# Optimization experiments

Hardware: AMD Instinct MI355X
Metric: run time of the kernel (lower is better)

## Reference

```python
import jax, jax.numpy as jnp
import numpy as np

N, E, D, H = 50000, 800000, 128, 128


def _uniform_param(key, shape, fan_in):
    bound = 1.0 / np.sqrt(fan_in)
    return jax.random.uniform(key, shape, jnp.float32, -bound, bound)


def setup_inputs() -> dict:
    key = jax.random.key(0)
    ks = jax.random.split(key, 12)
    x = jax.random.normal(ks[0], (N, D), jnp.float32)
    xedge = jax.random.randint(ks[1], (2, E), 0, N, jnp.int64)
    y = jax.random.randint(ks[2], (N,), 0, 2, jnp.int32).astype(bool)
    return {
        "x": x,
        "xedge": xedge,
        "y": y,
        "pretrain": 0,
        # SAGEConv layer 1 (in=D, out=H): lin_l (with bias) applied to mean aggr, lin_r (no bias) to self
        "W1l": _uniform_param(ks[3], (D, H), D),
        "b1l": _uniform_param(ks[4], (H,), D),
        "W1r": _uniform_param(ks[5], (D, H), D),
        # SAGEConv layer 2 (in=H, out=H)
        "W2l": _uniform_param(ks[6], (H, H), H),
        "b2l": _uniform_param(ks[7], (H,), H),
        "W2r": _uniform_param(ks[8], (H, H), H),
        # Decoder weight [H, H]
        "Wdec": _uniform_param(ks[9], (H, H), H),
    }


def sage_conv(h, src, dst, Wl, bl, Wr, num_nodes):
    # gather neighbor features along edges, mean-aggregate by destination
    msgs = h[src]                                            # [E, d]
    agg = jax.ops.segment_sum(msgs, dst, num_segments=num_nodes)
    cnt = jax.ops.segment_sum(jnp.ones((src.shape[0],), h.dtype), dst,
                              num_segments=num_nodes)
    mean = agg / jnp.maximum(cnt, 1.0)[:, None]              # [N, d]
    return mean @ Wl + bl + h @ Wr                           # [N, out]


def reference(x, xedge, y, pretrain, W1l, b1l, W1r, W2l, b2l, W2r, Wdec):
    src, dst = xedge[0], xedge[1]
    n = x.shape[0]
    # Encoder: SAGE = conv1 -> relu -> (dropout: eval identity) -> conv2
    h = jax.nn.relu(sage_conv(x, src, dst, W1l, b1l, W1r, n))
    emb = sage_conv(h, src, dst, W2l, b2l, W2r, n)           # [N, H]
    # Decoder
    dx = emb @ Wdec                                          # [N, H]
    # BCEWithLogits: pos nodes target 1, neg nodes target 0, mean within each group
    ym = y.astype(dx.dtype)                                  # [N]
    n_pos = jnp.sum(ym)
    n_neg = n - n_pos
    hdim = dx.shape[1]
    sp_pos = jax.nn.softplus(-dx)   # bce(logit, 1)
    sp_neg = jax.nn.softplus(dx)    # bce(logit, 0)
    l2 = jnp.sum(sp_pos * ym[:, None]) / (jnp.maximum(n_pos, 1.0) * hdim)
    l1 = jnp.sum(sp_neg * (1.0 - ym)[:, None]) / (jnp.maximum(n_neg, 1.0) * hdim)
    return (l1 + l2, emb)
```

## Files before the change

### kernel.cpp

```cpp
#include <hip/hip_runtime.h>
#include <hip/hip_bf16.h>

#define NDIM 128
#define SCAN_CHUNK 1024

typedef __attribute__((ext_vector_type(8))) short short8;
typedef __attribute__((ext_vector_type(4))) float f32x4;

__device__ __forceinline__ float bf2f(__hip_bfloat16 v) { return __bfloat162float(v); }

__device__ __forceinline__ float ldf(const void* p, long i, int f32) {
    return f32 ? ((const float*)p)[i] : bf2f(((const __hip_bfloat16*)p)[i]);
}
__device__ __forceinline__ void stf(void* p, long i, int f32, float v) {
    if (f32) ((float*)p)[i] = v;
    else     ((__hip_bfloat16*)p)[i] = __float2bfloat16(v);
}
__device__ __forceinline__ short f2bf(float v) {
    __hip_bfloat16 h = __float2bfloat16(v);
    short s;
    __builtin_memcpy(&s, &h, 2);
    return s;
}
__device__ __forceinline__ float bflo(unsigned u) { u <<= 16; float f; __builtin_memcpy(&f, &u, 4); return f; }
__device__ __forceinline__ float bfhi(unsigned u) { u &= 0xffff0000u; float f; __builtin_memcpy(&f, &u, 4); return f; }
__device__ __forceinline__ unsigned packbf(float a, float b) {
    unsigned la = (unsigned short)f2bf(a);
    unsigned hb = (unsigned short)f2bf(b);
    return (hb << 16) | la;
}
__device__ __forceinline__ int aswz(int m, int k) {
    return m * NDIM + ((((k >> 3) ^ (m & 7)) << 3) | (k & 7));
}
__device__ __forceinline__ int wswz(int m, int p) {
    return m * 64 + ((((p >> 2) ^ (m & 7)) << 2) | (p & 3));
}

__global__ void detect_kernel(const int* __restrict__ xedge32,
                              const unsigned int* __restrict__ yw,
                              const unsigned short* __restrict__ xh,
                              int* __restrict__ flags, int* __restrict__ cnt,
                              float* __restrict__ accum, int* __restrict__ npos, int N) {
    const int gid = blockIdx.x * 256 + threadIdx.x;
    for (int i = gid; i < N; i += gridDim.x * 256) cnt[i] = 0;
    if (gid == 0) { accum[0] = 0.f; accum[1] = 0.f; npos[0] = 0; }
    if (blockIdx.x == 0) {
        __shared__ int se, sy, scount;
        const int t = threadIdx.x;
        if (t == 0) { se = 1; sy = 0; scount = 0; }
        __syncthreads();
        for (int i = t; i < 512; i += 256)
            if (xedge32[2 * i + 1] != 0) se = 0;
        for (int i = t; i < 1024; i += 256)
            if (yw[i] > 1u) sy = 1;
        int c = 0;
        for (int i = t; i < 1024; i += 256) {
            int ex = (xh[2 * i] >> 7) & 0xFF;
            if (ex >= 100 && ex <= 150) c++;
        }
        atomicAdd(&scount, c);
        __syncthreads();
        if (t == 0) { flags[0] = se; flags[1] = sy; flags[2] = (scount < 900) ? 1 : 0; }
    }
}


__global__ void prep_kernel(const void* __restrict__ x,
                            const void* __restrict__ W1l, const void* __restrict__ b1l,
                            const void* __restrict__ W1r, const void* __restrict__ W2l,
                            const void* __restrict__ b2l, const void* __restrict__ W2r,
                            const void* __restrict__ Wd, const int* __restrict__ flags,
                            short* __restrict__ T1l, short* __restrict__ T1r,
                            short* __restrict__ T2l, short* __restrict__ T2r,
                            short* __restrict__ Td, float* __restrict__ b1c,
                            float* __restrict__ b2c, unsigned* __restrict__ xb,
                            const int* __restrict__ xedge, int E,
                            int* __restrict__ cnt, int N) {
    const int wf = flags[2];
    const long idx = (long)blockIdx.x * 256 + threadIdx.x;
    if (idx < E) {
        int d = flags[0] ? xedge[2 * (E + idx)] : xedge[E + idx];
        atomicAdd(&cnt[d], 1);
    }
    if (idx < NDIM * NDIM) {
        int k = (int)(idx >> 7), n = (int)(idx & 127);
        int o = n * NDIM + k;
        T1l[o] = f2bf(ldf(W1l, idx, wf));
        T1r[o] = f2bf(ldf(W1r, idx, wf));
        T2l[o] = f2bf(ldf(W2l, idx, wf));
        T2r[o] = f2bf(ldf(W2r, idx, wf));
        Td [o] = f2bf(ldf(Wd , idx, wf));
        if (idx < NDIM) { b1c[idx] = ldf(b1l, idx, wf); b2c[idx] = ldf(b2l, idx, wf); }
    } else {
        long p = idx - NDIM * NDIM;
        long np = (long)N * 64;
        if (p < np) {
            if (wf) {
                float2 v = ((const float2*)x)[p];
                xb[p] = packbf(v.x, v.y);
            } else {
                xb[p] = ((const unsigned*)x)[p];
            }
        }
    }
}


__global__ void scan_partial(const int* __restrict__ cnt, int* __restrict__ bsum, int N) {
    __shared__ int red[256];
    const int t = threadIdx.x;
    const long base = (long)blockIdx.x * SCAN_CHUNK + (long)t * 4;
    int s = 0;
#pragma unroll
    for (int i = 0; i < 4; ++i) { long idx = base + i; if (idx < N) s += cnt[idx]; }
    red[t] = s;
    __syncthreads();
    for (int off = 128; off >= 1; off >>= 1) {
        if (t < off) red[t] += red[t + off];
        __syncthreads();
    }
    if (t == 0) bsum[blockIdx.x] = red[0];
}

__global__ void scan_bsums(const int* __restrict__ bsum, int* __restrict__ boff,
                           int B, int* __restrict__ rowptr, int N) {
    __shared__ int part[1024];
    const int t = threadIdx.x;
    int v = (t < B) ? bsum[t] : 0;
    part[t] = v;
    __syncthreads();
    for (int off = 1; off < 1024; off <<= 1) {
        int u = (t >= off) ? part[t - off] : 0;
        __syncthreads();
        part[t] += u;
        __syncthreads();
    }
    if (t < B) boff[t] = part[t] - v;
    if (t == 1023) rowptr[N] = part[1023];
}

__global__ void scan_scatter(int* __restrict__ cnt, const int* __restrict__ boff,
                             int* __restrict__ rowptr, int N) {
    __shared__ int tsum[256];
    const int t = threadIdx.x;
    const long base = (long)blockIdx.x * SCAN_CHUNK + (long)t * 4;
    int loc[4];
    int s = 0;
#pragma unroll
    for (int i = 0; i < 4; ++i) {
        long idx = base + i;
        int c = (idx < N) ? cnt[idx] : 0;
        loc[i] = s;
        s += c;
    }
    tsum[t] = s;
    __syncthreads();
    for (int off = 1; off < 256; off <<= 1) {
        int u = (t >= off) ? tsum[t - off] : 0;
        __syncthreads();
        tsum[t] += u;
        __syncthreads();
    }
    const int texcl = tsum[t] - s;
    const int b0 = boff[blockIdx.x];
#pragma unroll
    for (int i = 0; i < 4; ++i) {
        long idx = base + i;
        if (idx < N) { rowptr[idx] = b0 + texcl + loc[i]; cnt[idx] = 0; }
    }
}

__global__ void fill_kernel(const int* __restrict__ xedge, int E,
                            const int* __restrict__ flags, const int* __restrict__ rowptr,
                            int* __restrict__ cur, int* __restrict__ col) {
    int e = blockIdx.x * blockDim.x + threadIdx.x;
    if (e >= E) return;
    const int e64 = flags[0];
    int s = e64 ? xedge[2 * e] : xedge[e];
    int d = e64 ? xedge[2 * (E + e)] : xedge[E + e];
    int p = rowptr[d] + atomicAdd(&cur[d], 1);
    col[p] = s;
}


template <bool RELU, int OUTMODE>
__global__ __launch_bounds__(256)
void layer_mfma(const unsigned* __restrict__ Xb, const int* __restrict__ rowptr,
                const int* __restrict__ col, const short* __restrict__ WlT,
                const float* __restrict__ biasc, const short* __restrict__ WrT,
                const short* __restrict__ WdT, const void* __restrict__ yv,
                const int* __restrict__ flags, void* __restrict__ outp,
                float* __restrict__ accum, int* __restrict__ npos, int N) {
    __shared__ short AS[2 * 32 * NDIM];
    __shared__ int ylds[32];
    __shared__ float redm[4][2];
    short* Ms = AS;
    short* Ss = AS + 32 * NDIM;
    unsigned* Msw = (unsigned*)Ms;
    unsigned* Ssw = (unsigned*)Ss;
    const int t = threadIdx.x;
    const int n0 = blockIdx.x * 32;
    const int wf = flags[2];

    if (OUTMODE == 1 && t < 32) {
        const int yb = flags[1];
        int n = n0 + t;
        int yn = -1;
        if (n < N)
            yn = yb ? (int)((const unsigned char*)yv)[n]
                    : (((const int*)yv)[n] != 0 ? 1 : 0);
        ylds[t] = yn;
    }

    {
        const int g = t >> 6, p = t & 63;
        for (int r = g; r < 32; r += 4) {
            int n = n0 + r;
            float m0 = 0.f, m1 = 0.f;
            unsigned su = 0;
            if (n < N) {
                int b = rowptr[n], e = rowptr[n + 1];
                int i = b;
                for (; i + 8 <= e; i += 8) {
                    unsigned u0 = Xb[(long)col[i    ] * 64 + p];
                    unsigned u1 = Xb[(long)col[i + 1] * 64 + p];
                    unsigned u2 = Xb[(long)col[i + 2] * 64 + p];
                    unsigned u3 = Xb[(long)col[i + 3] * 64 + p];
                    unsigned u4 = Xb[(long)col[i + 4] * 64 + p];
                    unsigned u5 = Xb[(long)col[i + 5] * 64 + p];
                    unsigned u6 = Xb[(long)col[i + 6] * 64 + p];
                    unsigned u7 = Xb[(long)col[i + 7] * 64 + p];
                    m0 += ((bflo(u0) + bflo(u1)) + (bflo(u2) + bflo(u3)))
                        + ((bflo(u4) + bflo(u5)) + (bflo(u6) + bflo(u7)));
                    m1 += ((bfhi(u0) + bfhi(u1)) + (bfhi(u2) + bfhi(u3)))
                        + ((bfhi(u4) + bfhi(u5)) + (bfhi(u6) + bfhi(u7)));
                }
                for (; i < e; ++i) {
                    unsigned u = Xb[(long)col[i] * 64 + p];
                    m0 += bflo(u);
                    m1 += bfhi(u);
                }
                float inv = 1.f / fmaxf((float)(e - b), 1.f);
                m0 *= inv; m1 *= inv;
                su = Xb[(long)n * 64 + p];
            }
            int wi = wswz(r, p);
            Msw[wi] = packbf(m0, m1);
            Ssw[wi] = su;
        }
    }
    __syncthreads();
    const int l = t & 63, w = t >> 6;
    const int quad = l >> 4, l15 = l & 15;
    const int wcol = w * 32;
    f32x4 acc[2][2] = {};
    for (int k0 = 0; k0 < NDIM; k0 += 32) {
        const int kc = k0 + quad * 8;
        short8 ams[2], ass[2], bl[2], br[2];
#pragma unroll
        for (int rt = 0; rt < 2; ++rt) {
            int m = rt * 16 + l15;
            ams[rt] = *(const short8*)&Ms[aswz(m, kc)];
            ass[rt] = *(const short8*)&Ss[aswz(m, kc)];
        }
#pragma unroll
        for (int ct = 0; ct < 2; ++ct) {
            int n = wcol + ct * 16 + l15;
            bl[ct] = *(const short8*)&WlT[n * NDIM + kc];
            br[ct] = *(const short8*)&WrT[n * NDIM + kc];
        }
#pragma unroll
        for (int rt = 0; rt < 2; ++rt)
#pragma unroll
            for (int ct = 0; ct < 2; ++ct) {
                acc[rt][ct] = __builtin_amdgcn_mfma_f32_16x16x32_bf16(
                    ams[rt], bl[ct], acc[rt][ct], 0, 0, 0);
                acc[rt][ct] = __builtin_amdgcn_mfma_f32_16x16x32_bf16(
                    ass[rt], br[ct], acc[rt][ct], 0, 0, 0);
            }
    }
    __syncthreads();

    if (OUTMODE == 0) {
#pragma unroll
        for (int ct = 0; ct < 2; ++ct) {
            int cg = wcol + ct * 16 + l15;
            float bv = biasc[cg];
#pragma unroll
            for (int rt = 0; rt < 2; ++rt)
#pragma unroll
                for (int reg = 0; reg < 4; ++reg) {
                    int row = rt * 16 + quad * 4 + reg;
                    float v = acc[rt][ct][reg] + bv;
                    if (RELU) v = fmaxf(v, 0.f);
                    Ms[row * NDIM + cg] = f2bf(v);
                }
        }
        __syncthreads();
        unsigned* ob = (unsigned*)outp;
        for (int idx = t; idx < 2048; idx += 256) {
            int r = idx >> 6;
            if (n0 + r < N) ob[(long)n0 * 64 + idx] = Msw[idx];
        }
    } else {
#pragma unroll
        for (int ct = 0; ct < 2; ++ct) {
            int cg = wcol + ct * 16 + l15;
            float bv = biasc[cg];
#pragma unroll
            for (int rt = 0; rt < 2; ++rt)
#pragma unroll
                for (int reg = 0; reg < 4; ++reg) {
                    int row = rt * 16 + quad * 4 + reg;
                    float v = acc[rt][ct][reg] + bv;
                    Ms[aswz(row, cg)] = f2bf(v);
                    int n = n0 + row;
                    if (n < N) {
                        if (wf) ((float*)outp)[1 + (long)n * NDIM + cg] = v;
                        else ((__hip_bfloat16*)outp)[1 + (long)n * NDIM + cg] =
                                 __float2bfloat16(v);
                    }
                }
        }
        __syncthreads();
        f32x4 acc2[2][2] = {};
        for (int k0 = 0; k0 < NDIM; k0 += 32) {
            const int kc = k0 + quad * 8;
            short8 a[2], b[2];
#pragma unroll
            for (int rt = 0; rt < 2; ++rt)
                a[rt] = *(const short8*)&Ms[aswz(rt * 16 + l15, kc)];
#pragma unroll
            for (int ct = 0; ct < 2; ++ct)
                b[ct] = *(const short8*)&WdT[(wcol + ct * 16 + l15) * NDIM + kc];
#pragma unroll
            for (int rt = 0; rt < 2; ++rt)
#pragma unroll
                for (int ct = 0; ct < 2; ++ct)
                    acc2[rt][ct] = __builtin_amdgcn_mfma_f32_16x16x32_bf16(
                        a[rt], b[ct], acc2[rt][ct], 0, 0, 0);
        }
        float lpos = 0.f, lneg = 0.f;
#pragma unroll
        for (int rt = 0; rt < 2; ++rt)
#pragma unroll
            for (int reg = 0; reg < 4; ++reg) {
                int row = rt * 16 + quad * 4 + reg;
                int yn = ylds[row];
                if (yn >= 0) {
#pragma unroll
                    for (int ct = 0; ct < 2; ++ct) {
                        float z = acc2[rt][ct][reg];
                        float L = log1pf(expf(-fabsf(z)));
                        if (yn) lpos += fmaxf(-z, 0.f) + L;
                        else    lneg += fmaxf(z, 0.f) + L;
                    }
                }
            }
#pragma unroll
        for (int off = 32; off >= 1; off >>= 1) {
            lpos += __shfl_down(lpos, off, 64);
            lneg += __shfl_down(lneg, off, 64);
        }
        if (l == 0) { redm[w][0] = lpos; redm[w][1] = lneg; }
        __syncthreads();
        if (t == 0) {
            atomicAdd(&accum[0], redm[0][0] + redm[1][0] + redm[2][0] + redm[3][0]);
            atomicAdd(&accum[1], redm[0][1] + redm[1][1] + redm[2][1] + redm[3][1]);
            int c = 0;
            for (int i = 0; i < 32; ++i) if (ylds[i] > 0) c++;
            if (c) atomicAdd(npos, c);
        }
    }
}

__global__ void finalize_kernel(const float* __restrict__ accum, const int* __restrict__ npos,
                                const int* __restrict__ flags, void* __restrict__ out, int N) {
    float np_ = (float)(*npos);
    float nn_ = (float)N - np_;
    float l2 = accum[0] / (fmaxf(np_, 1.f) * 128.f);
    float l1 = accum[1] / (fmaxf(nn_, 1.f) * 128.f);
    stf(out, 0, flags[2], l1 + l2);
}


extern "C" void kernel_launch(void* const* d_in, const int* in_sizes, int n_in,
                              void* d_out, int out_size, void* d_ws, size_t ws_size,
                              hipStream_t stream) {
    const void* x    = d_in[0];
    const int* xedge = (const int*)d_in[1];
    const void* y    = d_in[2];
    const void* W1l  = d_in[4];
    const void* b1l  = d_in[5];
    const void* W1r  = d_in[6];
    const void* W2l  = d_in[7];
    const void* b2l  = d_in[8];
    const void* W2r  = d_in[9];
    const void* Wdec = d_in[10];

    const int N = in_sizes[0] / NDIM;
    const int E = in_sizes[1] / 2;

    char* ws = (char*)d_ws;
    size_t off = 0;
    auto alloc = [&](size_t bytes) -> void* {
        void* p = ws + off;
        off = (off + bytes + 255) & ~(size_t)255;
        return p;
    };
    int*   flags  = (int*)alloc(64);
    float* accum  = (float*)alloc(64);
    int*   npos   = (int*)alloc(64);
    int*   bsum   = (int*)alloc(1024 * 4);
    int*   boff   = (int*)alloc(1024 * 4);
    int*   cnt    = (int*)alloc((size_t)N * 4);
    int*   rowptr = (int*)alloc((size_t)(N + 1) * 4);
    int*   col    = (int*)alloc((size_t)E * 4);
    unsigned* xb  = (unsigned*)alloc((size_t)N * 64 * 4);
    unsigned* hbuf = (unsigned*)alloc((size_t)N * 64 * 4);
    short* T1l = (short*)alloc(NDIM * NDIM * 2);
    short* T1r = (short*)alloc(NDIM * NDIM * 2);
    short* T2l = (short*)alloc(NDIM * NDIM * 2);
    short* T2r = (short*)alloc(NDIM * NDIM * 2);
    short* Td  = (short*)alloc(NDIM * NDIM * 2);
    float* b1c = (float*)alloc(NDIM * 4);
    float* b2c = (float*)alloc(NDIM * 4);

    const int zb = (N + 255) / 256;
    detect_kernel<<<zb, 256, 0, stream>>>(xedge, (const unsigned int*)y,
                                          (const unsigned short*)x, flags, cnt,
                                          accum, npos, N);
    const long prep_items = (long)NDIM * NDIM + (long)N * 64;
    prep_kernel<<<(int)((prep_items + 255) / 256), 256, 0, stream>>>(
        x, W1l, b1l, W1r, W2l, b2l, W2r, Wdec, flags,
        T1l, T1r, T2l, T2r, Td, b1c, b2c, xb, xedge, E, cnt, N);

    const int sb = (N + SCAN_CHUNK - 1) / SCAN_CHUNK;
    scan_partial<<<sb, 256, 0, stream>>>(cnt, bsum, N);
    scan_bsums<<<1, 1024, 0, stream>>>(bsum, boff, sb, rowptr, N);
    scan_scatter<<<sb, 256, 0, stream>>>(cnt, boff, rowptr, N);

    const int eb = (E + 255) / 256;
    fill_kernel<<<eb, 256, 0, stream>>>(xedge, E, flags, rowptr, cnt, col);

    const int nb32 = (N + 31) / 32;
    layer_mfma<true, 0><<<nb32, 256, 0, stream>>>(
        xb, rowptr, col, T1l, b1c, T1r, nullptr, nullptr, flags,
        hbuf, nullptr, nullptr, N);
    layer_mfma<false, 1><<<nb32, 256, 0, stream>>>(
        hbuf, rowptr, col, T2l, b2c, T2r, Td, y, flags,
        d_out, accum, npos, N);
    finalize_kernel<<<1, 1, 0, stream>>>(accum, npos, flags, d_out, N);
}
```

Before: 369.2 us.

## Batch neighbor gathers with wave-wide column prefetch and skip bf16 input copy

Each wave now loads up to 32 neighbor column indices in one vector load and broadcasts them with readlane, issuing 32 independent feature gathers per row (clamped duplicates for short rows) before reducing under a degree mask. The next row's rowptr and column indices are prefetched while the current row is being summed. When inputs are already bf16, the prep copy of x is skipped and the layer reads the raw input directly. The aim is more memory-level parallelism and less index-load latency in the aggregation, at the cost of higher register use and redundant loads for low-degree nodes.

After: 329.4 us. -10.8%, faster.

```diff
diff --git a/kernel.cpp b/kernel.cpp
--- a/kernel.cpp
+++ b/kernel.cpp
@@ -2,6 +2,7 @@
 #include <hip/hip_bf16.h>
 
 #define NDIM 128
+#define MROWS 32
 #define SCAN_CHUNK 1024
 
 typedef __attribute__((ext_vector_type(8))) short short8;
@@ -91,16 +92,12 @@
         T2r[o] = f2bf(ldf(W2r, idx, wf));
         Td [o] = f2bf(ldf(Wd , idx, wf));
         if (idx < NDIM) { b1c[idx] = ldf(b1l, idx, wf); b2c[idx] = ldf(b2l, idx, wf); }
-    } else {
+    } else if (wf) {
         long p = idx - NDIM * NDIM;
         long np = (long)N * 64;
         if (p < np) {
-            if (wf) {
-                float2 v = ((const float2*)x)[p];
-                xb[p] = packbf(v.x, v.y);
-            } else {
-                xb[p] = ((const unsigned*)x)[p];
-            }
+            float2 v = ((const float2*)x)[p];
+            xb[p] = packbf(v.x, v.y);
         }
     }
 }
@@ -185,24 +182,26 @@
 
 template <bool RELU, int OUTMODE>
 __global__ __launch_bounds__(256)
-void layer_mfma(const unsigned* __restrict__ Xb, const int* __restrict__ rowptr,
+void layer_mfma(const unsigned* __restrict__ Xb, const unsigned* __restrict__ Xraw,
+                const int* __restrict__ rowptr,
                 const int* __restrict__ col, const short* __restrict__ WlT,
                 const float* __restrict__ biasc, const short* __restrict__ WrT,
                 const short* __restrict__ WdT, const void* __restrict__ yv,
                 const int* __restrict__ flags, void* __restrict__ outp,
                 float* __restrict__ accum, int* __restrict__ npos, int N) {
-    __shared__ short AS[2 * 32 * NDIM];
-    __shared__ int ylds[32];
+    __shared__ short AS[2 * MROWS * NDIM];
+    __shared__ int ylds[MROWS];
     __shared__ float redm[4][2];
     short* Ms = AS;
-    short* Ss = AS + 32 * NDIM;
+    short* Ss = AS + MROWS * NDIM;
     unsigned* Msw = (unsigned*)Ms;
     unsigned* Ssw = (unsigned*)Ss;
     const int t = threadIdx.x;
-    const int n0 = blockIdx.x * 32;
+    const int n0 = blockIdx.x * MROWS;
     const int wf = flags[2];
-
-    if (OUTMODE == 1 && t < 32) {
+    const unsigned* __restrict__ X = wf ? Xb : Xraw;
+
+    if (OUTMODE == 1 && t < MROWS) {
         const int yb = flags[1];
         int n = n0 + t;
         int yn = -1;
@@ -213,40 +212,77 @@
     }
 
     {
-        const int g = t >> 6, p = t & 63;
-        for (int r = g; r < 32; r += 4) {
+        const int p = t & 63;
+        const int lj = t & 31;
+        const int g = __builtin_amdgcn_readfirstlane(t >> 6);
+        int r = g;
+        int b = 0, e = 0;
+        {
             int n = n0 + r;
+            if (n < N) {
+                b = __builtin_amdgcn_readfirstlane(rowptr[n]);
+                e = __builtin_amdgcn_readfirstlane(rowptr[n + 1]);
+            }
+        }
+        unsigned colv = 0;
+        if (e > b) {
+            int cl = b + lj;
+            if (cl >= e) cl = e - 1;
+            colv = (unsigned)col[cl];
+        }
+        for (int it = 0; it < 8; ++it, r += 4) {
+            const int n = n0 + r;
+            const int deg = e - b;
+            unsigned su = 0;
+            if (n < N) su = X[(long)n * 64 + p];
+            unsigned u[32];
+            if (deg > 0) {
+#pragma unroll
+                for (int j = 0; j < 32; ++j) {
+                    int c = __builtin_amdgcn_readlane((int)colv, j);
+                    u[j] = X[(long)c * 64 + p];
+                }
+            }
+            int bn = 0, en = 0;
+            unsigned colv_n = 0;
+            if (it < 7) {
+                int nn = n0 + r + 4;
+                if (nn < N) {
+                    bn = __builtin_amdgcn_readfirstlane(rowptr[nn]);
+                    en = __builtin_amdgcn_readfirstlane(rowptr[nn + 1]);
+                }
+                if (en > bn) {
+                    int cl = bn + lj;
+                    if (cl >= en) cl = en - 1;
+                    colv_n = (unsigned)col[cl];
+                }
+            }
             float m0 = 0.f, m1 = 0.f;
-            unsigned su = 0;
-            if (n < N) {
-                int b = rowptr[n], e = rowptr[n + 1];
-                int i = b;
-                for (; i + 8 <= e; i += 8) {
-                    unsigned u0 = Xb[(long)col[i    ] * 64 + p];
-                    unsigned u1 = Xb[(long)col[i + 1] * 64 + p];
-                    unsigned u2 = Xb[(long)col[i + 2] * 64 + p];
-                    unsigned u3 = Xb[(long)col[i + 3] * 64 + p];
-                    unsigned u4 = Xb[(long)col[i + 4] * 64 + p];
-                    unsigned u5 = Xb[(long)col[i + 5] * 64 + p];
-                    unsigned u6 = Xb[(long)col[i + 6] * 64 + p];
-                    unsigned u7 = Xb[(long)col[i + 7] * 64 + p];
-                    m0 += ((bflo(u0) + bflo(u1)) + (bflo(u2) + bflo(u3)))
-                        + ((bflo(u4) + bflo(u5)) + (bflo(u6) + bflo(u7)));
-                    m1 += ((bfhi(u0) + bfhi(u1)) + (bfhi(u2) + bfhi(u3)))
-                        + ((bfhi(u4) + bfhi(u5)) + (bfhi(u6) + bfhi(u7)));
-                }
-                for (; i < e; ++i) {
-                    unsigned u = Xb[(long)col[i] * 64 + p];
-                    m0 += bflo(u);
-                    m1 += bfhi(u);
-                }
-                float inv = 1.f / fmaxf((float)(e - b), 1.f);
+            if (deg > 0) {
+                float p0 = 0.f, p1 = 0.f, p2 = 0.f, p3 = 0.f;
+                float q0 = 0.f, q1 = 0.f, q2 = 0.f, q3 = 0.f;
+#pragma unroll
+                for (int j = 0; j < 32; j += 4) {
+                    if (j + 0 < deg) { p0 += bflo(u[j]);     q0 += bfhi(u[j]); }
+                    if (j + 1 < deg) { p1 += bflo(u[j + 1]); q1 += bfhi(u[j + 1]); }
+                    if (j + 2 < deg) { p2 += bflo(u[j + 2]); q2 += bfhi(u[j + 2]); }
+                    if (j + 3 < deg) { p3 += bflo(u[j + 3]); q3 += bfhi(u[j + 3]); }
+                }
+                m0 = (p0 + p1) + (p2 + p3);
+                m1 = (q0 + q1) + (q2 + q3);
+                for (int i = b + 32; i < e; ++i) {
+                    int c = __builtin_amdgcn_readfirstlane(col[i]);
+                    unsigned uu = X[(long)c * 64 + p];
+                    m0 += bflo(uu);
+                    m1 += bfhi(uu);
+                }
+                float inv = 1.f / (float)deg;
                 m0 *= inv; m1 *= inv;
-                su = Xb[(long)n * 64 + p];
             }
             int wi = wswz(r, p);
             Msw[wi] = packbf(m0, m1);
             Ssw[wi] = su;
+            b = bn; e = en; colv = colv_n;
         }
     }
     __syncthreads();
@@ -298,7 +334,7 @@
         }
         __syncthreads();
         unsigned* ob = (unsigned*)outp;
-        for (int idx = t; idx < 2048; idx += 256) {
+        for (int idx = t; idx < MROWS * 64; idx += 256) {
             int r = idx >> 6;
             if (n0 + r < N) ob[(long)n0 * 64 + idx] = Msw[idx];
         }
@@ -368,7 +404,7 @@
             atomicAdd(&accum[0], redm[0][0] + redm[1][0] + redm[2][0] + redm[3][0]);
             atomicAdd(&accum[1], redm[0][1] + redm[1][1] + redm[2][1] + redm[3][1]);
             int c = 0;
-            for (int i = 0; i < 32; ++i) if (ylds[i] > 0) c++;
+            for (int i = 0; i < MROWS; ++i) if (ylds[i] > 0) c++;
             if (c) atomicAdd(npos, c);
         }
     }
@@ -443,12 +479,12 @@
     const int eb = (E + 255) / 256;
     fill_kernel<<<eb, 256, 0, stream>>>(xedge, E, flags, rowptr, cnt, col);
 
-    const int nb32 = (N + 31) / 32;
-    layer_mfma<true, 0><<<nb32, 256, 0, stream>>>(
-        xb, rowptr, col, T1l, b1c, T1r, nullptr, nullptr, flags,
-        hbuf, nullptr, nullptr, N);
-    layer_mfma<false, 1><<<nb32, 256, 0, stream>>>(
-        hbuf, rowptr, col, T2l, b2c, T2r, Td, y, flags,
+    const int nbM = (N + MROWS - 1) / MROWS;
+    layer_mfma<true, 0><<<nbM, 256, 0, stream>>>(
+        xb, (const unsigned*)x, rowptr, col, T1l, b1c, T1r, nullptr, nullptr,
+        flags, hbuf, nullptr, nullptr, N);
+    layer_mfma<false, 1><<<nbM, 256, 0, stream>>>(
+        hbuf, hbuf, rowptr, col, T2l, b2c, T2r, Td, y, flags,
         d_out, accum, npos, N);
     finalize_kernel<<<1, 1, 0, stream>>>(accum, npos, flags, d_out, N);
 }
```
